# Kernel optimization log

Measured on AMD Instinct MI355X. Metric: run time of the kernel, lower is better.

Reference implementation:

```python
import jax, jax.numpy as jnp
import numpy as np

B = 512        # batch
L = 2000       # number of timestamps
D = 16         # data_dim (control channels)
H = 128        # hidden_dim (CDE state)
WIDTH = 256    # vf_hidden_dim
LBL = 10       # label_dim
N_STEPS = 500  # (t1 - t0) / dt0 with t in [0,1], dt0 = 0.002


def _linear_init(key, out_dim, in_dim):
    lim = 1.0 / np.sqrt(in_dim)
    kw, kb = jax.random.split(key)
    w = jax.random.uniform(kw, (out_dim, in_dim), minval=-lim, maxval=lim, dtype=jnp.float32)
    b = jax.random.uniform(kb, (out_dim,), minval=-lim, maxval=lim, dtype=jnp.float32)
    return w, b


def setup_inputs() -> dict:
    key = jax.random.key(0)
    ks = jax.random.split(key, 8)
    ts = jnp.arange(L, dtype=jnp.float32) / (L - 1)          # uniform grid on [0, 1]
    # cubic interpolation coeffs, diffrax order (d, c, b, a) per interval
    coeffs = jax.random.normal(ks[0], (B, 4, L - 1, D), dtype=jnp.float32) * 0.1
    x0 = jax.random.normal(ks[1], (B, D), dtype=jnp.float32)
    W1, b1 = _linear_init(ks[2], WIDTH, H)
    W2, b2 = _linear_init(ks[3], WIDTH, WIDTH)
    W3, b3 = _linear_init(ks[4], H * D, WIDTH)
    Wl1, bl1 = _linear_init(ks[5], H, D)
    Wl2, bl2 = _linear_init(ks[6], LBL, H)
    return dict(ts=ts, coeffs=coeffs, x0=x0, W1=W1, b1=b1, W2=W2, b2=b2,
                W3=W3, b3=b3, Wl1=Wl1, bl1=bl1, Wl2=Wl2, bl2=bl2)


def _cde_forward(ts, coeffs, x0, W1, b1, W2, b2, W3, b3, Wl1, bl1, Wl2, bl2):
    # vector field: MLP H -> WIDTH -> WIDTH -> H*D, relu hidden, tanh final
    def vf(y):  # y: (B, H) -> (B, H, D)
        h = jax.nn.relu(y @ W1.T + b1)
        h = jax.nn.relu(h @ W2.T + b2)
        o = jnp.tanh(h @ W3.T + b3)
        return o.reshape(B, H, D)

    d_, c_, b_ = coeffs[:, 0], coeffs[:, 1], coeffs[:, 2]  # each (B, L-1, D)

    def dXdt(t):  # derivative of cubic spline at scalar time t -> (B, D)
        idx = jnp.clip(jnp.searchsorted(ts, t, side='right') - 1, 0, L - 2)
        tau = t - ts[idx]
        return b_[:, idx] + (2.0 * tau) * c_[:, idx] + (3.0 * tau * tau) * d_[:, idx]

    def f(t, y):  # controlled ODE vector field: (B, H)
        return jnp.einsum('bhd,bd->bh', vf(y), dXdt(t))

    t0, t1 = ts[0], ts[-1]
    dt = (t1 - t0) / N_STEPS
    y0 = x0 @ Wl1.T + bl1  # linear1, (B, H)

    def heun_step(y, k):
        t = t0 + k.astype(jnp.float32) * dt
        k1 = f(t, y)
        k2 = f(t + dt, y + dt * k1)
        y_next = y + (0.5 * dt) * (k1 + k2)
        return y_next, None

    yT, _ = jax.lax.scan(heun_step, y0, jnp.arange(N_STEPS))
    return jax.nn.softmax(yT @ Wl2.T + bl2, axis=-1)  # classification head


def reference(ts, coeffs, x0, W1, b1, W2, b2, W3, b3, Wl1, bl1, Wl2, bl2):
    return _cde_forward(ts, coeffs, x0, W1, b1, W2, b2, W3, b3, Wl1, bl1, Wl2, bl2)
```

## Files before the change

### kernel.cpp

```cpp
#include <hip/hip_runtime.h>

#define BB 512
#define LL 2000
#define DD 16
#define HH 128
#define WD 256
#define NLBL 10
#define NSTEPS 500
#define G 16
#define NSL 8
#define NGRP (BB / G)
#define NWG (NGRP * NSL)
#define NTHR 512

typedef __bf16 bf16x8 __attribute__((ext_vector_type(8)));
typedef float f32x4 __attribute__((ext_vector_type(4)));

__device__ __forceinline__ float aload(const float* p) {
  return __hip_atomic_load(p, __ATOMIC_RELAXED, __HIP_MEMORY_SCOPE_AGENT);
}
__device__ __forceinline__ void astore(float* p, float v) {
  __hip_atomic_store(p, v, __ATOMIC_RELAXED, __HIP_MEMORY_SCOPE_AGENT);
}
__device__ __forceinline__ unsigned int aloadu(const unsigned int* p) {
  return __hip_atomic_load(p, __ATOMIC_RELAXED, __HIP_MEMORY_SCOPE_AGENT);
}

__device__ __forceinline__ unsigned short f2bf(float f) {
  unsigned int u = __float_as_uint(f);
  u += 0x7FFFu + ((u >> 16) & 1u);
  return (unsigned short)(u >> 16);
}

__device__ __forceinline__ int swz(int r, int c) {
  return r * WD + ((((c >> 3) ^ (r & 7)) << 3) | (c & 7));
}

__device__ __forceinline__ bf16x8 ldfrag(const unsigned short* buf, int row, int chunk) {
  return *reinterpret_cast<const bf16x8*>(buf + row * WD + ((chunk ^ (row & 7)) << 3));
}

__device__ unsigned char enc_e4m3(float x) {
  float ax = fabsf(x);
  unsigned char sg = (unsigned char)((__float_as_uint(x) >> 24) & 0x80u);
  if (ax > 448.f) ax = 448.f;
  if (ax < 0.001953125f) {
    int m = (int)rintf(ax * 512.f);
    return sg | (unsigned char)m;
  }
  unsigned int u = __float_as_uint(ax);
  unsigned int r = u + 0x7FFFFu + ((u >> 20) & 1u);
  r &= 0xFFF00000u;
  int e = (int)(r >> 23) - 127;
  if (e < -6) {
    int m = (int)rintf(ax * 512.f);
    if (m >= 8) return sg | 0x08;
    return sg | (unsigned char)m;
  }
  if (e > 8) return sg | 0x7E;
  unsigned int m = (r >> 20) & 7u;
  return sg | (unsigned char)(((e + 7) << 3) | m);
}

__device__ __forceinline__ unsigned int pk4_fp8(float a, float b, float c, float d) {
#if __has_builtin(__builtin_amdgcn_cvt_pk_fp8_f32)
  int w0 = __builtin_amdgcn_cvt_pk_fp8_f32(a, b, 0, false);
  w0 = __builtin_amdgcn_cvt_pk_fp8_f32(c, d, w0, true);
  return (unsigned int)w0;
#else
  return (unsigned int)enc_e4m3(a) | ((unsigned int)enc_e4m3(b) << 8) |
         ((unsigned int)enc_e4m3(c) << 16) | ((unsigned int)enc_e4m3(d) << 24);
#endif
}

struct __align__(16) SM {
  uint2 q8l[16 * 512];
  float Y[G][HH];
  float K1[G][HH];
  unsigned short X[G * WD];
  unsigned short Hb[G * WD];
  unsigned long long X8w[G * 33];
  float dx[2][G][DD];
  float b1[WD], b2[WD];
  float2 sb3[256];
  float tsl[LL];
  float tau_tab[2 * NSTEPS];
  unsigned short idx_tab[2 * NSTEPS];
  float logits[G * NLBL];
};

__global__ void prep_scale(const float* __restrict__ W3, float* __restrict__ w3s) {
  int row = blockIdx.x * 4 + (threadIdx.x >> 6);
  int lane = threadIdx.x & 63;
  const float* wr = W3 + (size_t)row * WD;
  float m = 0.f;
#pragma unroll
  for (int i = 0; i < 4; ++i) m = fmaxf(m, fabsf(wr[lane + 64 * i]));
#pragma unroll
  for (int off = 32; off >= 1; off >>= 1) m = fmaxf(m, __shfl_xor(m, off));
  if (lane == 0) w3s[row] = fmaxf(m, 1e-30f) * (1.0f / 240.0f);
}

__global__ void prep_pack(const float* __restrict__ W3, const float* __restrict__ w3s,
                          uint2* __restrict__ q8) {
  int o = blockIdx.x * blockDim.x + threadIdx.x;
  int lane = o & 63, s = (o >> 6) & 7, nt = o >> 9;
  int row = nt * 16 + (lane & 15);
  int k0 = s * 32 + ((lane >> 4) << 3);
  float inv = 1.0f / w3s[row];
  const float* src = W3 + (size_t)row * WD + k0;
  unsigned int lo = 0, hi = 0;
#pragma unroll
  for (int j = 0; j < 4; ++j) lo |= (unsigned int)enc_e4m3(src[j] * inv) << (8 * j);
#pragma unroll
  for (int j = 0; j < 4; ++j) hi |= (unsigned int)enc_e4m3(src[4 + j] * inv) << (8 * j);
  q8[o] = make_uint2(lo, hi);
}

__global__ __launch_bounds__(NTHR, 2) void cde_main(
    const float* __restrict__ ts, const float* __restrict__ coeffs,
    const float* __restrict__ x0,
    const float* __restrict__ b1g, const float* __restrict__ b2g, const float* __restrict__ b3g,
    const float* __restrict__ Wl1, const float* __restrict__ bl1,
    const float* __restrict__ Wl2, const float* __restrict__ bl2,
    const float* __restrict__ W1, const float* __restrict__ W2,
    const uint2* __restrict__ q8g, const float* __restrict__ w3s,
    float* __restrict__ exA, float* __restrict__ exB,
    unsigned int* __restrict__ flags,
    float* __restrict__ out) {
  extern __shared__ char smraw[];
  SM& sm = *reinterpret_cast<SM*>(smraw);
  const int tid = threadIdx.x;
  const int bid = blockIdx.x;
  const int g = bid & 31, s16 = bid >> 5;
  const int gb = g * G;
  const int w = tid >> 6, lane = tid & 63;
  const int row16 = lane & 15, kg = lane >> 4;

  const float ts0 = ts[0];
  const float dt = (ts[LL - 1] - ts0) / (float)NSTEPS;
  const float hdt = 0.5f * dt;

  for (int i = tid; i < LL; i += NTHR) sm.tsl[i] = ts[i];
  for (int i = tid; i < WD; i += NTHR) { sm.b1[i] = b1g[i]; sm.b2[i] = b2g[i]; }
  for (int i = tid; i < 256; i += NTHR) {
    int rg = s16 * 256 + i;
    sm.sb3[i] = make_float2(w3s[rg], b3g[rg]);
  }
  for (int i = tid; i < 16 * 512; i += NTHR) sm.q8l[i] = q8g[s16 * 8192 + i];

  for (int i = tid; i < G * HH; i += NTHR) {
    int r = i >> 7, h = i & (HH - 1);
    float s = bl1[h];
    const float* xr = x0 + (size_t)(gb + r) * DD;
    const float* wr = Wl1 + (size_t)h * DD;
#pragma unroll
    for (int d = 0; d < DD; ++d) s += xr[d] * wr[d];
    sm.Y[r][h] = s;
    sm.X[swz(r, h)] = f2bf(s);
  }

  bf16x8 w1f[2][4], w2f[2][8];
#pragma unroll
  for (int tt = 0; tt < 2; ++tt) {
    int n = (w + tt * 8) * 16 + row16;
#pragma unroll
    for (int s = 0; s < 4; ++s) {
      bf16x8 v;
#pragma unroll
      for (int e = 0; e < 8; ++e)
        v[e] = __builtin_bit_cast(__bf16, f2bf(W1[(size_t)n * HH + (s * 4 + kg) * 8 + e]));
      w1f[tt][s] = v;
    }
#pragma unroll
    for (int s = 0; s < 8; ++s) {
      bf16x8 v;
#pragma unroll
      for (int e = 0; e < 8; ++e)
        v[e] = __builtin_bit_cast(__bf16, f2bf(W2[(size_t)n * WD + (s * 4 + kg) * 8 + e]));
      w2f[tt][s] = v;
    }
  }
  __syncthreads();

  for (int e = tid; e < 2 * NSTEPS; e += NTHR) {
    int kk = e >> 1;
    float t = ts0 + (float)kk * dt;
    if (e & 1) t = t + dt;
    int lo = 0, hi = LL;
    while (lo < hi) { int m = (lo + hi) >> 1; if (sm.tsl[m] <= t) lo = m + 1; else hi = m; }
    int idx = lo - 1;
    if (idx < 0) idx = 0;
    if (idx > LL - 2) idx = LL - 2;
    sm.idx_tab[e] = (unsigned short)idx;
    sm.tau_tab[e] = t - sm.tsl[idx];
  }
  __syncthreads();

  {
    int which = tid >> 8, rr = (tid >> 4) & 15, d = tid & 15;
    int idx = sm.idx_tab[which];
    float tau = sm.tau_tab[which];
    const float* cb = coeffs + ((size_t)(gb + rr) * 4 * (LL - 1) + idx) * DD + d;
    float c0 = cb[0];
    float c1 = cb[(size_t)(LL - 1) * DD];
    float c2 = cb[(size_t)2 * (LL - 1) * DD];
    sm.dx[which][rr][d] = c2 + 2.0f * tau * c1 + 3.0f * tau * tau * c0;
  }

  {
    unsigned int* ic = &flags[1024];
    __syncthreads();
    if (tid == 0) {
      atomicAdd(ic, 1u);
      while (aloadu(ic) < NWG) __builtin_amdgcn_s_sleep(1);
    }
    __syncthreads();
  }

  float pc0 = 0.f, pc1 = 0.f, pc2 = 0.f, ptau = 0.f;
  unsigned int nb = 0;
  unsigned int* gctr = &flags[g * 32];

  auto PH = [&](float* exDst, int stage) {
    {
      bf16x8 a[4];
#pragma unroll
      for (int s = 0; s < 4; ++s) a[s] = ldfrag(sm.X, row16, s * 4 + kg);
#pragma unroll
      for (int tt = 0; tt < 2; ++tt) {
        const int n = (w + tt * 8) * 16 + row16;
        f32x4 acc = {0.f, 0.f, 0.f, 0.f};
#pragma unroll
        for (int s = 0; s < 4; ++s)
          acc = __builtin_amdgcn_mfma_f32_16x16x32_bf16(a[s], w1f[tt][s], acc, 0, 0, 0);
#pragma unroll
        for (int v = 0; v < 4; ++v)
          sm.Hb[swz(kg * 4 + v, n)] = f2bf(fmaxf(acc[v] + sm.b1[n], 0.f));
      }
    }
    __syncthreads();

    {
      bf16x8 hb[8];
#pragma unroll
      for (int s = 0; s < 8; ++s) hb[s] = ldfrag(sm.Hb, row16, s * 4 + kg);
      unsigned int* x8u = reinterpret_cast<unsigned int*>(sm.X8w);
#pragma unroll
      for (int tt = 0; tt < 2; ++tt) {
        const int T = w + tt * 8;
        f32x4 acc = {0.f, 0.f, 0.f, 0.f};
#pragma unroll
        for (int s = 0; s < 8; ++s)
          acc = __builtin_amdgcn_mfma_f32_16x16x32_bf16(w2f[tt][s], hb[s], acc, 0, 0, 0);
        const int nbi = T * 16 + kg * 4;
        float o0 = fmaxf(acc[0] + sm.b2[nbi + 0], 0.f);
        float o1 = fmaxf(acc[1] + sm.b2[nbi + 1], 0.f);
        float o2 = fmaxf(acc[2] + sm.b2[nbi + 2], 0.f);
        float o3 = fmaxf(acc[3] + sm.b2[nbi + 3], 0.f);
        x8u[row16 * 66 + T * 4 + kg] = pk4_fp8(o0, o1, o2, o3);
      }
    }
    __syncthreads();

    {
      long b8[8];
#pragma unroll
      for (int s = 0; s < 8; ++s)
        b8[s] = __builtin_bit_cast(long, sm.X8w[row16 * 33 + s * 4 + kg]);
      const float4 dx4 = *reinterpret_cast<const float4*>(&sm.dx[stage][row16][kg * 4]);
#pragma unroll
      for (int j = 0; j < 2; ++j) {
        const int ntl = w + j * 8;
        const uint2* wp = sm.q8l + ntl * 512 + lane;
        f32x4 acc = {0.f, 0.f, 0.f, 0.f};
#pragma unroll
        for (int s = 0; s < 8; ++s)
          acc = __builtin_amdgcn_mfma_f32_16x16x32_fp8_fp8(
              __builtin_bit_cast(long, wp[s * 64]), b8[s], acc, 0, 0, 0);
        float psum = 0.f;
#pragma unroll
        for (int v = 0; v < 4; ++v) {
          const float2 sb = sm.sb3[ntl * 16 + kg * 4 + v];
          float o = acc[v] * sb.x + sb.y;
          float e2 = __expf(2.0f * o);
          float T = 1.0f - 2.0f / (e2 + 1.0f);
          psum += T * (v == 0 ? dx4.x : v == 1 ? dx4.y : v == 2 ? dx4.z : dx4.w);
        }
        psum += __shfl_xor(psum, 16);
        psum += __shfl_xor(psum, 32);
        if (kg == 0) astore(exDst + (size_t)(gb + row16) * HH + (s16 * 16 + ntl), psum);
      }
    }
  };

  auto arrive = [&]() {
    __syncthreads();
    if (tid == 0) atomicAdd(gctr, 1u);
  };
  auto waitc = [&](unsigned int tgt) {
    if (tid == 0)
      while (aloadu(gctr) < tgt) __builtin_amdgcn_s_sleep(1);
    __syncthreads();
  };

  for (int k = 0; k < NSTEPS; ++k) {
    {
      int which = tid >> 8, rr = (tid >> 4) & 15, d = tid & 15;
      int e = 2 * (k + 1) + which;
      if (e > 2 * NSTEPS - 1) e = 2 * NSTEPS - 1;
      int idx = sm.idx_tab[e];
      ptau = sm.tau_tab[e];
      const float* cb = coeffs + ((size_t)(gb + rr) * 4 * (LL - 1) + idx) * DD + d;
      pc0 = cb[0];
      pc1 = cb[(size_t)(LL - 1) * DD];
      pc2 = cb[(size_t)2 * (LL - 1) * DD];
    }
    PH(exA, 0);
    arrive();
    waitc(++nb * NSL);
    {
      int r = tid >> 5, c = (tid & 31) << 2;
      const float* src = exA + (size_t)(gb + r) * HH + c;
      float f0 = aload(src), f1 = aload(src + 1), f2 = aload(src + 2), f3 = aload(src + 3);
      sm.K1[r][c] = f0; sm.K1[r][c + 1] = f1; sm.K1[r][c + 2] = f2; sm.K1[r][c + 3] = f3;
      sm.X[swz(r, c)] = f2bf(sm.Y[r][c] + dt * f0);
      sm.X[swz(r, c + 1)] = f2bf(sm.Y[r][c + 1] + dt * f1);
      sm.X[swz(r, c + 2)] = f2bf(sm.Y[r][c + 2] + dt * f2);
      sm.X[swz(r, c + 3)] = f2bf(sm.Y[r][c + 3] + dt * f3);
    }
    __syncthreads();

    PH(exB, 1);
    arrive();
    waitc(++nb * NSL);
    {
      int r = tid >> 5, c = (tid & 31) << 2;
      const float* src = exB + (size_t)(gb + r) * HH + c;
      float f0 = aload(src), f1 = aload(src + 1), f2 = aload(src + 2), f3 = aload(src + 3);
      float y0n = sm.Y[r][c] + hdt * (sm.K1[r][c] + f0);
      float y1n = sm.Y[r][c + 1] + hdt * (sm.K1[r][c + 1] + f1);
      float y2n = sm.Y[r][c + 2] + hdt * (sm.K1[r][c + 2] + f2);
      float y3n = sm.Y[r][c + 3] + hdt * (sm.K1[r][c + 3] + f3);
      sm.Y[r][c] = y0n; sm.Y[r][c + 1] = y1n; sm.Y[r][c + 2] = y2n; sm.Y[r][c + 3] = y3n;
      sm.X[swz(r, c)] = f2bf(y0n);
      sm.X[swz(r, c + 1)] = f2bf(y1n);
      sm.X[swz(r, c + 2)] = f2bf(y2n);
      sm.X[swz(r, c + 3)] = f2bf(y3n);
      int which = tid >> 8, rr = (tid >> 4) & 15, d = tid & 15;
      sm.dx[which][rr][d] = pc2 + 2.0f * ptau * pc1 + 3.0f * ptau * ptau * pc0;
    }
    __syncthreads();
  }

  if (s16 == 0) {
    if (tid < G * NLBL) {
      int r = tid / NLBL, c = tid % NLBL;
      float s = bl2[c];
      const float* wr = Wl2 + (size_t)c * HH;
#pragma unroll 4
      for (int h = 0; h < HH; ++h) s += sm.Y[r][h] * wr[h];
      sm.logits[tid] = s;
    }
    __syncthreads();
    if (tid < G) {
      float mx = -1e30f;
#pragma unroll
      for (int c = 0; c < NLBL; ++c) mx = fmaxf(mx, sm.logits[tid * NLBL + c]);
      float e[NLBL], sum = 0.f;
#pragma unroll
      for (int c = 0; c < NLBL; ++c) { e[c] = expf(sm.logits[tid * NLBL + c] - mx); sum += e[c]; }
      float inv = 1.0f / sum;
#pragma unroll
      for (int c = 0; c < NLBL; ++c) out[(size_t)(gb + tid) * NLBL + c] = e[c] * inv;
    }
  }
}

extern "C" void kernel_launch(void* const* d_in, const int* in_sizes, int n_in,
                              void* d_out, int out_size, void* d_ws, size_t ws_size,
                              hipStream_t stream) {
  (void)in_sizes; (void)n_in; (void)out_size; (void)ws_size;
  const float* ts = (const float*)d_in[0];
  const float* coeffs = (const float*)d_in[1];
  const float* x0 = (const float*)d_in[2];
  const float* W1 = (const float*)d_in[3];
  const float* b1 = (const float*)d_in[4];
  const float* W2 = (const float*)d_in[5];
  const float* b2 = (const float*)d_in[6];
  const float* W3 = (const float*)d_in[7];
  const float* b3 = (const float*)d_in[8];
  const float* Wl1 = (const float*)d_in[9];
  const float* bl1 = (const float*)d_in[10];
  const float* Wl2 = (const float*)d_in[11];
  const float* bl2 = (const float*)d_in[12];

  char* ws = (char*)d_ws;
  uint2* q8 = (uint2*)ws;
  float* exA = (float*)ws;
  float* exB = (float*)(ws + 262144);
  float* w3s = (float*)(ws + 524288);
  unsigned int* flags = (unsigned int*)(ws + 532480);

  static_assert(sizeof(SM) <= 160 * 1024, "LDS overflow");
  hipFuncSetAttribute(reinterpret_cast<const void*>(cde_main),
                      hipFuncAttributeMaxDynamicSharedMemorySize, (int)sizeof(SM));

  hipMemsetAsync(flags, 0, 8192, stream);
  prep_scale<<<512, 256, 0, stream>>>(W3, w3s);
  prep_pack<<<256, 256, 0, stream>>>(W3, w3s, q8);

  float* outp = (float*)d_out;
  void* args[] = {&ts, &coeffs, &x0, &b1, &b2, &b3, &Wl1, &bl1, &Wl2, &bl2,
                  &W1, &W2, &q8, &w3s, &exA, &exB, &flags, &outp};
  hipLaunchCooperativeKernel(reinterpret_cast<const void*>(cde_main), dim3(NWG), dim3(NTHR),
                             args, (unsigned int)sizeof(SM), stream);
}
```

Before: 3.384 ms.

## Replace atomic group counter with per-workgroup flags and vectorize epilogue LDS stores

Replaces the shared atomicAdd counter per batch group with one flag per workgroup, each written with a plain atomic store. A whole wavefront polls its eight peer flags in parallel. The first-layer MFMA operands are swapped so that each lane writes packed bf16 pairs to the hidden buffer as one 8-byte store instead of four scalar stores. The fp8 buffer stride is padded from 33 to 35 and the bias and scale loads are vectorized. The change aims to cut contention on the atomic counter and LDS store traffic in a latency-bound loop that runs 1000 times, in exchange for more flag memory and more polling loads.

```diff
diff --git a/kernel.cpp b/kernel.cpp
--- a/kernel.cpp
+++ b/kernel.cpp
@@ -12,6 +12,7 @@
 #define NGRP (BB / G)
 #define NWG (NGRP * NSL)
 #define NTHR 512
+#define X8S 35
 
 typedef __bf16 bf16x8 __attribute__((ext_vector_type(8)));
 typedef float f32x4 __attribute__((ext_vector_type(4)));
@@ -24,12 +25,18 @@
 }
 __device__ __forceinline__ unsigned int aloadu(const unsigned int* p) {
   return __hip_atomic_load(p, __ATOMIC_RELAXED, __HIP_MEMORY_SCOPE_AGENT);
+}
+__device__ __forceinline__ void astoreu(unsigned int* p, unsigned int v) {
+  __hip_atomic_store(p, v, __ATOMIC_RELAXED, __HIP_MEMORY_SCOPE_AGENT);
 }
 
 __device__ __forceinline__ unsigned short f2bf(float f) {
   unsigned int u = __float_as_uint(f);
   u += 0x7FFFu + ((u >> 16) & 1u);
   return (unsigned short)(u >> 16);
+}
+__device__ __forceinline__ unsigned int pk2bf(float a, float b) {
+  return (unsigned int)f2bf(a) | ((unsigned int)f2bf(b) << 16);
 }
 
 __device__ __forceinline__ int swz(int r, int c) {
@@ -79,7 +86,7 @@
   float K1[G][HH];
   unsigned short X[G * WD];
   unsigned short Hb[G * WD];
-  unsigned long long X8w[G * 33];
+  unsigned long long X8w[G * X8S];
   float dx[2][G][DD];
   float b1[WD], b2[WD];
   float2 sb3[256];
@@ -209,7 +216,7 @@
   }
 
   {
-    unsigned int* ic = &flags[1024];
+    unsigned int* ic = &flags[8192];
     __syncthreads();
     if (tid == 0) {
       atomicAdd(ic, 1u);
@@ -220,45 +227,53 @@
 
   float pc0 = 0.f, pc1 = 0.f, pc2 = 0.f, ptau = 0.f;
   unsigned int nb = 0;
-  unsigned int* gctr = &flags[g * 32];
+  unsigned int* myflag = &flags[(g * 8 + s16) * 32];
+  const unsigned int* peerflag = &flags[(g * 8 + (lane & 7)) * 32];
 
   auto PH = [&](float* exDst, int stage) {
     {
       bf16x8 a[4];
 #pragma unroll
       for (int s = 0; s < 4; ++s) a[s] = ldfrag(sm.X, row16, s * 4 + kg);
-#pragma unroll
-      for (int tt = 0; tt < 2; ++tt) {
-        const int n = (w + tt * 8) * 16 + row16;
-        f32x4 acc = {0.f, 0.f, 0.f, 0.f};
-#pragma unroll
-        for (int s = 0; s < 4; ++s)
-          acc = __builtin_amdgcn_mfma_f32_16x16x32_bf16(a[s], w1f[tt][s], acc, 0, 0, 0);
-#pragma unroll
-        for (int v = 0; v < 4; ++v)
-          sm.Hb[swz(kg * 4 + v, n)] = f2bf(fmaxf(acc[v] + sm.b1[n], 0.f));
-      }
-    }
-    __syncthreads();
-
-    {
-      bf16x8 hb[8];
-#pragma unroll
-      for (int s = 0; s < 8; ++s) hb[s] = ldfrag(sm.Hb, row16, s * 4 + kg);
-      unsigned int* x8u = reinterpret_cast<unsigned int*>(sm.X8w);
 #pragma unroll
       for (int tt = 0; tt < 2; ++tt) {
         const int T = w + tt * 8;
         f32x4 acc = {0.f, 0.f, 0.f, 0.f};
 #pragma unroll
+        for (int s = 0; s < 4; ++s)
+          acc = __builtin_amdgcn_mfma_f32_16x16x32_bf16(w1f[tt][s], a[s], acc, 0, 0, 0);
+        const int h1b = T * 16 + kg * 4;
+        const float4 b14 = *reinterpret_cast<const float4*>(&sm.b1[h1b]);
+        float o0 = fmaxf(acc[0] + b14.x, 0.f);
+        float o1 = fmaxf(acc[1] + b14.y, 0.f);
+        float o2 = fmaxf(acc[2] + b14.z, 0.f);
+        float o3 = fmaxf(acc[3] + b14.w, 0.f);
+        int cp = ((2 * T + (kg >> 1)) ^ (row16 & 7));
+        uint2* dst = reinterpret_cast<uint2*>(sm.Hb + row16 * WD + cp * 8 + (kg & 1) * 4);
+        *dst = make_uint2(pk2bf(o0, o1), pk2bf(o2, o3));
+      }
+    }
+    __syncthreads();
+
+    {
+      bf16x8 hb[8];
+#pragma unroll
+      for (int s = 0; s < 8; ++s) hb[s] = ldfrag(sm.Hb, row16, s * 4 + kg);
+      unsigned int* x8u = reinterpret_cast<unsigned int*>(sm.X8w);
+#pragma unroll
+      for (int tt = 0; tt < 2; ++tt) {
+        const int T = w + tt * 8;
+        f32x4 acc = {0.f, 0.f, 0.f, 0.f};
+#pragma unroll
         for (int s = 0; s < 8; ++s)
           acc = __builtin_amdgcn_mfma_f32_16x16x32_bf16(w2f[tt][s], hb[s], acc, 0, 0, 0);
         const int nbi = T * 16 + kg * 4;
-        float o0 = fmaxf(acc[0] + sm.b2[nbi + 0], 0.f);
-        float o1 = fmaxf(acc[1] + sm.b2[nbi + 1], 0.f);
-        float o2 = fmaxf(acc[2] + sm.b2[nbi + 2], 0.f);
-        float o3 = fmaxf(acc[3] + sm.b2[nbi + 3], 0.f);
-        x8u[row16 * 66 + T * 4 + kg] = pk4_fp8(o0, o1, o2, o3);
+        const float4 b24 = *reinterpret_cast<const float4*>(&sm.b2[nbi]);
+        float o0 = fmaxf(acc[0] + b24.x, 0.f);
+        float o1 = fmaxf(acc[1] + b24.y, 0.f);
+        float o2 = fmaxf(acc[2] + b24.z, 0.f);
+        float o3 = fmaxf(acc[3] + b24.w, 0.f);
+        x8u[row16 * (2 * X8S) + T * 4 + kg] = pk4_fp8(o0, o1, o2, o3);
       }
     }
     __syncthreads();
@@ -267,7 +282,7 @@
       long b8[8];
 #pragma unroll
       for (int s = 0; s < 8; ++s)
-        b8[s] = __builtin_bit_cast(long, sm.X8w[row16 * 33 + s * 4 + kg]);
+        b8[s] = __builtin_bit_cast(long, sm.X8w[row16 * X8S + s * 4 + kg]);
       const float4 dx4 = *reinterpret_cast<const float4*>(&sm.dx[stage][row16][kg * 4]);
 #pragma unroll
       for (int j = 0; j < 2; ++j) {
@@ -278,14 +293,22 @@
         for (int s = 0; s < 8; ++s)
           acc = __builtin_amdgcn_mfma_f32_16x16x32_fp8_fp8(
               __builtin_bit_cast(long, wp[s * 64]), b8[s], acc, 0, 0, 0);
+        const float4* sb4 = reinterpret_cast<const float4*>(&sm.sb3[ntl * 16 + kg * 4]);
+        float4 sba = sb4[0], sbb = sb4[1];
         float psum = 0.f;
-#pragma unroll
-        for (int v = 0; v < 4; ++v) {
-          const float2 sb = sm.sb3[ntl * 16 + kg * 4 + v];
-          float o = acc[v] * sb.x + sb.y;
+        {
+          float o = acc[0] * sba.x + sba.y;
           float e2 = __expf(2.0f * o);
-          float T = 1.0f - 2.0f / (e2 + 1.0f);
-          psum += T * (v == 0 ? dx4.x : v == 1 ? dx4.y : v == 2 ? dx4.z : dx4.w);
+          psum += (1.0f - 2.0f / (e2 + 1.0f)) * dx4.x;
+          o = acc[1] * sba.z + sba.w;
+          e2 = __expf(2.0f * o);
+          psum += (1.0f - 2.0f / (e2 + 1.0f)) * dx4.y;
+          o = acc[2] * sbb.x + sbb.y;
+          e2 = __expf(2.0f * o);
+          psum += (1.0f - 2.0f / (e2 + 1.0f)) * dx4.z;
+          o = acc[3] * sbb.z + sbb.w;
+          e2 = __expf(2.0f * o);
+          psum += (1.0f - 2.0f / (e2 + 1.0f)) * dx4.w;
         }
         psum += __shfl_xor(psum, 16);
         psum += __shfl_xor(psum, 32);
@@ -296,11 +319,17 @@
 
   auto arrive = [&]() {
     __syncthreads();
-    if (tid == 0) atomicAdd(gctr, 1u);
+    if (tid == 0) astoreu(myflag, nb);
   };
   auto waitc = [&](unsigned int tgt) {
-    if (tid == 0)
-      while (aloadu(gctr) < tgt) __builtin_amdgcn_s_sleep(1);
+    if (w == 0) {
+      bool done;
+      do {
+        bool ok = (lane >= 8) || (aloadu(peerflag) >= tgt);
+        done = __all(ok);
+        if (!done) __builtin_amdgcn_s_sleep(1);
+      } while (!done);
+    }
     __syncthreads();
   };
 
@@ -317,8 +346,9 @@
       pc2 = cb[(size_t)2 * (LL - 1) * DD];
     }
     PH(exA, 0);
+    ++nb;
     arrive();
-    waitc(++nb * NSL);
+    waitc(nb);
     {
       int r = tid >> 5, c = (tid & 31) << 2;
       const float* src = exA + (size_t)(gb + r) * HH + c;
@@ -332,8 +362,9 @@
     __syncthreads();
 
     PH(exB, 1);
+    ++nb;
     arrive();
-    waitc(++nb * NSL);
+    waitc(nb);
     {
       int r = tid >> 5, c = (tid & 31) << 2;
       const float* src = exB + (size_t)(gb + r) * HH + c;
@@ -406,7 +437,7 @@
   hipFuncSetAttribute(reinterpret_cast<const void*>(cde_main),
                       hipFuncAttributeMaxDynamicSharedMemorySize, (int)sizeof(SM));
 
-  hipMemsetAsync(flags, 0, 8192, stream);
+  hipMemsetAsync(flags, 0, 36864, stream);
   prep_scale<<<512, 256, 0, stream>>>(W3, w3s);
   prep_pack<<<256, 256, 0, stream>>>(W3, w3s, q8);
 
```

New measurement: 4.044 ms. 1.2x slower.
